# Kernel optimization log

Hardware: AMD Instinct MI355X
Metric: run time of the kernel (lower is better)

Reference implementation:

```python
import jax, jax.numpy as jnp
import numpy as np

B, L, HID = 16, 2048, 4096
CQ, CKV = 1536, 512
H, DH, DR = 32, 128, 64


def setup_inputs() -> dict:
    key = jax.random.key(0)
    ks = jax.random.split(key, 12)
    w = lambda k, shp: jax.random.normal(k, shp, dtype=jnp.float32) * 0.02
    return {
        'hidden_states': jax.random.normal(ks[0], (B, 1, HID), dtype=jnp.float32),
        'cached_cKV': jax.random.normal(ks[1], (B, L, CKV), dtype=jnp.float32),
        'cached_kR': jax.random.normal(ks[2], (B, L, H * DR), dtype=jnp.float32),
        'W_DQ': w(ks[3], (HID, CQ)),
        'W_DKV': w(ks[4], (HID, CKV)),
        'W_UQ_C': w(ks[5], (CQ, H * DH)),
        'W_UQ_R': w(ks[6], (CQ, H * DR)),
        'W_KR': w(ks[7], (HID, H * DR)),
        'W_UK_C': w(ks[8], (CKV, H * DH)),
        'W_UV_C': w(ks[9], (CKV, H * DH)),
        'W_O': w(ks[10], (H * DH, HID)),
    }


def _apply_rope(x, pos):
    # x: (B, S, H, D); standard rotate-pairs RoPE with base 10000
    D = x.shape[-1]
    inv_freq = 1.0 / (10000.0 ** (jnp.arange(0, D, 2, dtype=jnp.float32) / D))
    ang = pos.astype(jnp.float32)[:, None] * inv_freq[None, :]  # (S, D/2)
    cos = jnp.cos(ang)[None, :, None, :]
    sin = jnp.sin(ang)[None, :, None, :]
    x1, x2 = x[..., ::2], x[..., 1::2]
    r1 = x1 * cos - x2 * sin
    r2 = x1 * sin + x2 * cos
    return jnp.stack([r1, r2], axis=-1).reshape(x.shape)


def reference(hidden_states, cached_cKV, cached_kR, W_DQ, W_DKV, W_UQ_C, W_UQ_R, W_KR, W_UK_C, W_UV_C, W_O):
    b, seq_len, _ = hidden_states.shape  # seq_len == 1 (decode)
    # compressed query + up-projections
    cQ_t = jnp.einsum('bsh,hq->bsq', hidden_states, W_DQ)
    qC_t = jnp.einsum('bsq,qc->bsc', cQ_t, W_UQ_C)
    qR_t = jnp.einsum('bsq,qr->bsr', cQ_t, W_UQ_R)
    kR_t = jnp.einsum('bsh,hr->bsr', hidden_states, W_KR)
    # RoPE on rope-dim heads (single decode token -> position 0)
    pos = jnp.arange(seq_len)
    qR_t = _apply_rope(qR_t.reshape(b, seq_len, H, DR), pos).reshape(b, seq_len, H * DR)
    kR_t = _apply_rope(kR_t.reshape(b, seq_len, H, DR), pos).reshape(b, seq_len, H * DR)
    # compressed KV for new token
    cKV_t = jnp.einsum('bsh,hv->bsv', hidden_states, W_DKV)
    # absorption trick: fold W_UK_C into the query
    qC_eff = jnp.einsum('bsc,ck->bsk', qC_t, W_UK_C.T)  # (B,1,CKV)
    score_Cprefix = jnp.einsum('bsk,bLk->bsL', qC_eff, cached_cKV)
    new_token_score_C = jnp.einsum('bsk,bsk->bs', qC_eff, cKV_t)[:, None]
    score_Rprefix = jnp.einsum('bsr,bLr->bsL', qR_t, cached_kR)
    new_token_score_R = jnp.einsum('bsr,bsr->bs', qR_t, kR_t)[:, None]
    scores = jnp.concatenate([score_Cprefix + score_Rprefix,
                              new_token_score_C + new_token_score_R], axis=-1)
    scores = scores / jnp.sqrt(jnp.float32(DH + DR))
    attn_probs = jax.nn.softmax(scores, axis=-1)  # (B,1,L+1)
    # absorbed value/output projection
    W_VO = jnp.einsum('kv,vc->kc', W_UV_C, W_O)  # (CKV, HID)
    prefix_value = jnp.einsum('bLk,kc->bLc', cached_cKV, W_VO)
    prefix_value_agg = jnp.einsum('bsl,blc->bsc', attn_probs[..., :-1], prefix_value)
    new_value = jnp.einsum('bsk,kc->bsc', cKV_t, W_VO)
    output = prefix_value_agg + attn_probs[..., -1:] * new_value
    new_cached_cKV = jnp.concatenate([cached_cKV, cKV_t], axis=1)
    new_cached_kR = jnp.concatenate([cached_kR, kR_t], axis=1)
    return output, new_cached_cKV, new_cached_kR
```

## Files before the change

kernel.cpp:

```cpp
#include <hip/hip_runtime.h>

#define HIDN 4096
#define CQD  1536
#define CKVD 512
#define NH   32
#define DH   128
#define DR   64
#define BATCH 16
#define SEQL 2048
#define HDR  (NH*DR)
#define HDH  (NH*DH)
#define LP1  (SEQL+1)

__device__ __forceinline__ void gemm16_core(
    const float* __restrict__ A, int K, int k0, int KC,
    const float* __restrict__ W, int ldW, int wcol,
    float* __restrict__ C, int ldC, int ccol,
    float* sA, int tid) {
    for (int i = tid; i < KC * 16; i += 256) {
        int k = i >> 4, b = i & 15;
        sA[i] = A[b * K + k0 + k];
    }
    __syncthreads();
    float2 acc[16];
#pragma unroll
    for (int b = 0; b < 16; ++b) acc[b] = make_float2(0.f, 0.f);
    const float* Wp = W + (size_t)k0 * ldW + wcol;
    const float4* sA4 = (const float4*)sA;
#pragma unroll 4
    for (int k = 0; k < KC; ++k) {
        float2 w = *(const float2*)(Wp + (size_t)k * ldW);
        float av[16];
        *(float4*)&av[0]  = sA4[k * 4 + 0];
        *(float4*)&av[4]  = sA4[k * 4 + 1];
        *(float4*)&av[8]  = sA4[k * 4 + 2];
        *(float4*)&av[12] = sA4[k * 4 + 3];
#pragma unroll
        for (int b = 0; b < 16; ++b) {
            acc[b].x += av[b] * w.x;
            acc[b].y += av[b] * w.y;
        }
    }
#pragma unroll
    for (int b = 0; b < 16; ++b) {
        atomicAdd(&C[b * ldC + ccol],     acc[b].x);
        atomicAdd(&C[b * ldC + ccol + 1], acc[b].y);
    }
}

__global__ __launch_bounds__(256) void proj_hidden(
    const float* __restrict__ hidden,
    const float* __restrict__ W_DQ, const float* __restrict__ W_DKV,
    const float* __restrict__ W_KR,
    float* __restrict__ cQ, float* __restrict__ cKV_t, float* __restrict__ kR_t) {
    const int KC = 128;
    __shared__ float sA[16 * KC];
    int nb = blockIdx.x;
    const float* W; float* C; int ld; int col0;
    if (nb < 3)      { W = W_DQ;  C = cQ;    ld = CQD;  col0 = nb * 512; }
    else if (nb < 4) { W = W_DKV; C = cKV_t; ld = CKVD; col0 = 0; }
    else             { W = W_KR;  C = kR_t;  ld = HDR;  col0 = (nb - 4) * 512; }
    int cn = col0 + threadIdx.x * 2;
    gemm16_core(hidden, HIDN, blockIdx.y * KC, KC, W, ld, cn, C, ld, cn, sA, threadIdx.x);
}

__global__ __launch_bounds__(256) void proj_cq(
    const float* __restrict__ cQ,
    const float* __restrict__ W_UQ_C, const float* __restrict__ W_UQ_R,
    float* __restrict__ qC, float* __restrict__ qR) {
    const int KC = 64;
    __shared__ float sA[16 * KC];
    int nb = blockIdx.x;
    const float* W; float* C; int ld; int col0;
    if (nb < 8) { W = W_UQ_C; C = qC; ld = HDH; col0 = nb * 512; }
    else        { W = W_UQ_R; C = qR; ld = HDR; col0 = (nb - 8) * 512; }
    int cn = col0 + threadIdx.x * 2;
    gemm16_core(cQ, CQD, blockIdx.y * KC, KC, W, ld, cn, C, ld, cn, sA, threadIdx.x);
}

template <int KC>
__global__ __launch_bounds__(256) void gemm16_gen(
    const float* __restrict__ A, const float* __restrict__ W,
    float* __restrict__ C, int K, int N) {
    __shared__ float sA[16 * KC];
    int cn = blockIdx.x * 512 + threadIdx.x * 2;
    gemm16_core(A, K, blockIdx.y * KC, KC, W, N, cn, C, N, cn, sA, threadIdx.x);
}

__global__ __launch_bounds__(256) void qceff_v2(
    const float* __restrict__ qC, const float* __restrict__ WUK,
    float* __restrict__ qC_eff) {
    int wave = threadIdx.x >> 6, lane = threadIdx.x & 63;
    int k = blockIdx.x * 2 + (wave >> 1);
    int half = wave & 1;
    const float4* wrow = (const float4*)(WUK + (size_t)k * HDH + half * 2048);
    const float4* q4   = (const float4*)(qC + half * 2048);
    float acc[16];
#pragma unroll
    for (int b = 0; b < 16; ++b) acc[b] = 0.f;
#pragma unroll
    for (int it = 0; it < 8; ++it) {
        int c4 = it * 64 + lane;
        float4 w = wrow[c4];
#pragma unroll
        for (int b = 0; b < 16; ++b) {
            float4 q = q4[b * 1024 + c4];
            acc[b] += q.x * w.x + q.y * w.y + q.z * w.z + q.w * w.w;
        }
    }
#pragma unroll
    for (int b = 0; b < 16; ++b) {
        float v = acc[b];
#pragma unroll
        for (int off = 32; off > 0; off >>= 1) v += __shfl_down(v, off, 64);
        if (lane == 0) atomicAdd(&qC_eff[b * CKVD + k], v);
    }
}

__global__ __launch_bounds__(256) void score_copy_kernel(
    const float* __restrict__ cached_cKV, const float* __restrict__ cached_kR,
    const float* __restrict__ cKV_t, const float* __restrict__ kR_t,
    const float* __restrict__ qC_eff, const float* __restrict__ qR,
    float* __restrict__ out_cKV, float* __restrict__ out_kR,
    float* __restrict__ scores) {
    int l = blockIdx.x;
    int b = blockIdx.y;
    int tid = threadIdx.x;
    int wave = tid >> 6, lane = tid & 63;
    const float4* ckv_row;
    const float4* kr_row;
    if (l < SEQL) {
        ckv_row = (const float4*)(cached_cKV + ((size_t)b * SEQL + l) * CKVD);
        kr_row  = (const float4*)(cached_kR  + ((size_t)b * SEQL + l) * HDR);
    } else {
        ckv_row = (const float4*)(cKV_t + b * CKVD);
        kr_row  = (const float4*)(kR_t + b * HDR);
    }
    float4* oc  = (float4*)(out_cKV + ((size_t)b * LP1 + l) * CKVD);
    float4* okr = (float4*)(out_kR  + ((size_t)b * LP1 + l) * HDR);
    const float4* qc4 = (const float4*)(qC_eff + b * CKVD);
    const float4* qr4 = (const float4*)(qR + b * HDR);
    float acc = 0.f;
    if (tid < 128) {
        float4 v = ckv_row[tid];
        float4 q = qc4[tid];
        acc += v.x * q.x + v.y * q.y + v.z * q.z + v.w * q.w;
        oc[tid] = v;
    }
#pragma unroll
    for (int j = 0; j < 2; ++j) {
        int i = tid + j * 256;
        float4 v = kr_row[i];
        float4 q = qr4[i];
        acc += v.x * q.x + v.y * q.y + v.z * q.z + v.w * q.w;
        okr[i] = v;
    }
#pragma unroll
    for (int off = 32; off > 0; off >>= 1) acc += __shfl_down(acc, off, 64);
    __shared__ float sRed[4];
    if (lane == 0) sRed[wave] = acc;
    __syncthreads();
    if (tid == 0)
        scores[b * LP1 + l] =
            (sRed[0] + sRed[1] + sRed[2] + sRed[3]) * 0.07216878364870323f;
}

__global__ __launch_bounds__(256) void softmax_kernel(
    const float* __restrict__ scores, float* __restrict__ probs) {
    int b = blockIdx.x;
    int tid = threadIdx.x;
    __shared__ float red[256];
    float m = -1e30f;
    for (int i = tid; i < LP1; i += 256) m = fmaxf(m, scores[b * LP1 + i]);
    red[tid] = m; __syncthreads();
    for (int s = 128; s > 0; s >>= 1) {
        if (tid < s) red[tid] = fmaxf(red[tid], red[tid + s]);
        __syncthreads();
    }
    m = red[0]; __syncthreads();
    float sum = 0.f;
    for (int i = tid; i < LP1; i += 256) sum += __expf(scores[b * LP1 + i] - m);
    red[tid] = sum; __syncthreads();
    for (int s = 128; s > 0; s >>= 1) {
        if (tid < s) red[tid] += red[tid + s];
        __syncthreads();
    }
    float inv = 1.0f / red[0];
    for (int i = tid; i < LP1; i += 256)
        probs[b * LP1 + i] = __expf(scores[b * LP1 + i] - m) * inv;
}

__global__ __launch_bounds__(256) void ctx_kernel(
    const float* __restrict__ out_cKV, const float* __restrict__ probs,
    float* __restrict__ ctx) {
    int b = blockIdx.y;
    int tid = threadIdx.x;
    int c4 = tid & 127, sub = tid >> 7;
    int l0 = blockIdx.x * 128;
    int lend = l0 + 128; if (lend > LP1) lend = LP1;
    float4 acc = make_float4(0.f, 0.f, 0.f, 0.f);
    for (int l = l0 + sub; l < lend; l += 2) {
        float p = probs[b * LP1 + l];
        const float4* row = (const float4*)(out_cKV + ((size_t)b * LP1 + l) * CKVD);
        float4 v = row[c4];
        acc.x += p * v.x; acc.y += p * v.y; acc.z += p * v.z; acc.w += p * v.w;
    }
    float* dst = ctx + b * CKVD + c4 * 4;
    atomicAdd(dst + 0, acc.x);
    atomicAdd(dst + 1, acc.y);
    atomicAdd(dst + 2, acc.z);
    atomicAdd(dst + 3, acc.w);
}

extern "C" void kernel_launch(void* const* d_in, const int* in_sizes, int n_in,
                              void* d_out, int out_size, void* d_ws, size_t ws_size,
                              hipStream_t stream) {
    const float* hidden     = (const float*)d_in[0];
    const float* cached_cKV = (const float*)d_in[1];
    const float* cached_kR  = (const float*)d_in[2];
    const float* W_DQ   = (const float*)d_in[3];
    const float* W_DKV  = (const float*)d_in[4];
    const float* W_UQ_C = (const float*)d_in[5];
    const float* W_UQ_R = (const float*)d_in[6];
    const float* W_KR   = (const float*)d_in[7];
    const float* W_UK_C = (const float*)d_in[8];
    const float* W_UV_C = (const float*)d_in[9];
    const float* W_O    = (const float*)d_in[10];

    float* out     = (float*)d_out;
    float* out_cKV = out + BATCH * HDH;
    float* out_kR  = out_cKV + (size_t)BATCH * LP1 * CKVD;

    float* ws      = (float*)d_ws;
    float* cQ      = ws;
    float* cKV_t   = cQ + BATCH * CQD;
    float* kR_t    = cKV_t + BATCH * CKVD;
    float* qC      = kR_t + BATCH * HDR;
    float* qR      = qC + BATCH * HDH;
    float* qC_eff  = qR + BATCH * HDR;
    float* ctx     = qC_eff + BATCH * CKVD;
    float* tbuf    = ctx + BATCH * CKVD;
    float* scores  = tbuf + BATCH * HDH;
    float* probs   = scores + BATCH * LP1;
    size_t n_ws_floats = (size_t)(probs + BATCH * LP1 - ws);

    hipMemsetAsync(d_ws, 0, n_ws_floats * sizeof(float), stream);
    hipMemsetAsync(d_out, 0, (size_t)BATCH * HDH * sizeof(float), stream);

    dim3 blk(256);
    proj_hidden<<<dim3(8, HIDN / 128), blk, 0, stream>>>(
        hidden, W_DQ, W_DKV, W_KR, cQ, cKV_t, kR_t);
    proj_cq<<<dim3(12, CQD / 64), blk, 0, stream>>>(cQ, W_UQ_C, W_UQ_R, qC, qR);
    qceff_v2<<<dim3(CKVD / 2), blk, 0, stream>>>(qC, W_UK_C, qC_eff);
    score_copy_kernel<<<dim3(LP1, BATCH), blk, 0, stream>>>(
        cached_cKV, cached_kR, cKV_t, kR_t, qC_eff, qR, out_cKV, out_kR, scores);
    softmax_kernel<<<dim3(BATCH), blk, 0, stream>>>(scores, probs);
    ctx_kernel<<<dim3((LP1 + 127) / 128, BATCH), blk, 0, stream>>>(out_cKV, probs, ctx);
    gemm16_gen<32><<<dim3(HDH / 512, CKVD / 32), blk, 0, stream>>>(
        ctx, W_UV_C, tbuf, CKVD, HDH);
    gemm16_gen<128><<<dim3(HIDN / 512, HDH / 128), blk, 0, stream>>>(
        tbuf, W_O, out, HDH, HIDN);
}
```

Baseline: 790.2 us.

## Rework decode MLA kernels: narrower GEMM tiles, nontemporal copies, fused softmax into ctx

```diff
diff --git a/kernel.cpp b/kernel.cpp
--- a/kernel.cpp
+++ b/kernel.cpp
@@ -12,40 +12,43 @@
 #define HDH  (NH*DH)
 #define LP1  (SEQL+1)
 
-__device__ __forceinline__ void gemm16_core(
+typedef float f32x4 __attribute__((ext_vector_type(4)));
+
+__device__ __forceinline__ f32x4 nt_load4(const float* p) {
+    return __builtin_nontemporal_load((const f32x4*)p);
+}
+__device__ __forceinline__ void nt_store4(float* p, f32x4 v) {
+    __builtin_nontemporal_store(v, (f32x4*)p);
+}
+
+__device__ __forceinline__ void gemm16_col_core(
     const float* __restrict__ A, int K, int k0, int KC,
-    const float* __restrict__ W, int ldW, int wcol,
-    float* __restrict__ C, int ldC, int ccol,
+    const float* __restrict__ W, int ldW, int col,
+    float* __restrict__ C, int ldC,
     float* sA, int tid) {
     for (int i = tid; i < KC * 16; i += 256) {
         int k = i >> 4, b = i & 15;
         sA[i] = A[b * K + k0 + k];
     }
     __syncthreads();
-    float2 acc[16];
-#pragma unroll
-    for (int b = 0; b < 16; ++b) acc[b] = make_float2(0.f, 0.f);
-    const float* Wp = W + (size_t)k0 * ldW + wcol;
+    float acc[16];
+#pragma unroll
+    for (int b = 0; b < 16; ++b) acc[b] = 0.f;
+    const float* Wp = W + (size_t)k0 * ldW + col;
     const float4* sA4 = (const float4*)sA;
 #pragma unroll 4
     for (int k = 0; k < KC; ++k) {
-        float2 w = *(const float2*)(Wp + (size_t)k * ldW);
+        float w = Wp[(size_t)k * ldW];
         float av[16];
         *(float4*)&av[0]  = sA4[k * 4 + 0];
         *(float4*)&av[4]  = sA4[k * 4 + 1];
         *(float4*)&av[8]  = sA4[k * 4 + 2];
         *(float4*)&av[12] = sA4[k * 4 + 3];
 #pragma unroll
-        for (int b = 0; b < 16; ++b) {
-            acc[b].x += av[b] * w.x;
-            acc[b].y += av[b] * w.y;
-        }
-    }
-#pragma unroll
-    for (int b = 0; b < 16; ++b) {
-        atomicAdd(&C[b * ldC + ccol],     acc[b].x);
-        atomicAdd(&C[b * ldC + ccol + 1], acc[b].y);
-    }
+        for (int b = 0; b < 16; ++b) acc[b] += av[b] * w;
+    }
+#pragma unroll
+    for (int b = 0; b < 16; ++b) atomicAdd(&C[b * ldC + col], acc[b]);
 }
 
 __global__ __launch_bounds__(256) void proj_hidden(
@@ -57,11 +60,11 @@
     __shared__ float sA[16 * KC];
     int nb = blockIdx.x;
     const float* W; float* C; int ld; int col0;
-    if (nb < 3)      { W = W_DQ;  C = cQ;    ld = CQD;  col0 = nb * 512; }
-    else if (nb < 4) { W = W_DKV; C = cKV_t; ld = CKVD; col0 = 0; }
-    else             { W = W_KR;  C = kR_t;  ld = HDR;  col0 = (nb - 4) * 512; }
-    int cn = col0 + threadIdx.x * 2;
-    gemm16_core(hidden, HIDN, blockIdx.y * KC, KC, W, ld, cn, C, ld, cn, sA, threadIdx.x);
+    if (nb < 6)      { W = W_DQ;  C = cQ;    ld = CQD;  col0 = nb * 256; }
+    else if (nb < 8) { W = W_DKV; C = cKV_t; ld = CKVD; col0 = (nb - 6) * 256; }
+    else             { W = W_KR;  C = kR_t;  ld = HDR;  col0 = (nb - 8) * 256; }
+    gemm16_col_core(hidden, HIDN, blockIdx.y * KC, KC, W, ld,
+                    col0 + threadIdx.x, C, ld, sA, threadIdx.x);
 }
 
 __global__ __launch_bounds__(256) void proj_cq(
@@ -72,10 +75,10 @@
     __shared__ float sA[16 * KC];
     int nb = blockIdx.x;
     const float* W; float* C; int ld; int col0;
-    if (nb < 8) { W = W_UQ_C; C = qC; ld = HDH; col0 = nb * 512; }
-    else        { W = W_UQ_R; C = qR; ld = HDR; col0 = (nb - 8) * 512; }
-    int cn = col0 + threadIdx.x * 2;
-    gemm16_core(cQ, CQD, blockIdx.y * KC, KC, W, ld, cn, C, ld, cn, sA, threadIdx.x);
+    if (nb < 16) { W = W_UQ_C; C = qC; ld = HDH; col0 = nb * 256; }
+    else         { W = W_UQ_R; C = qR; ld = HDR; col0 = (nb - 16) * 256; }
+    gemm16_col_core(cQ, CQD, blockIdx.y * KC, KC, W, ld,
+                    col0 + threadIdx.x, C, ld, sA, threadIdx.x);
 }
 
 template <int KC>
@@ -83,24 +86,23 @@
     const float* __restrict__ A, const float* __restrict__ W,
     float* __restrict__ C, int K, int N) {
     __shared__ float sA[16 * KC];
-    int cn = blockIdx.x * 512 + threadIdx.x * 2;
-    gemm16_core(A, K, blockIdx.y * KC, KC, W, N, cn, C, N, cn, sA, threadIdx.x);
-}
-
-__global__ __launch_bounds__(256) void qceff_v2(
+    int col = blockIdx.x * 256 + threadIdx.x;
+    gemm16_col_core(A, K, blockIdx.y * KC, KC, W, N, col, C, N, sA, threadIdx.x);
+}
+
+__global__ __launch_bounds__(256) void qceff_v3(
     const float* __restrict__ qC, const float* __restrict__ WUK,
     float* __restrict__ qC_eff) {
-    int wave = threadIdx.x >> 6, lane = threadIdx.x & 63;
-    int k = blockIdx.x * 2 + (wave >> 1);
-    int half = wave & 1;
-    const float4* wrow = (const float4*)(WUK + (size_t)k * HDH + half * 2048);
-    const float4* q4   = (const float4*)(qC + half * 2048);
+    int k = blockIdx.x;
+    int tid = threadIdx.x, wave = tid >> 6, lane = tid & 63;
+    const float4* wrow = (const float4*)(WUK + (size_t)k * HDH);
+    const float4* q4   = (const float4*)qC;
     float acc[16];
 #pragma unroll
     for (int b = 0; b < 16; ++b) acc[b] = 0.f;
 #pragma unroll
-    for (int it = 0; it < 8; ++it) {
-        int c4 = it * 64 + lane;
+    for (int it = 0; it < 4; ++it) {
+        int c4 = wave * 256 + it * 64 + lane;
         float4 w = wrow[c4];
 #pragma unroll
         for (int b = 0; b < 16; ++b) {
@@ -108,13 +110,50 @@
             acc[b] += q.x * w.x + q.y * w.y + q.z * w.z + q.w * w.w;
         }
     }
+    __shared__ float sRed[64];
 #pragma unroll
     for (int b = 0; b < 16; ++b) {
         float v = acc[b];
 #pragma unroll
         for (int off = 32; off > 0; off >>= 1) v += __shfl_down(v, off, 64);
-        if (lane == 0) atomicAdd(&qC_eff[b * CKVD + k], v);
-    }
+        if (lane == 0) sRed[wave * 16 + b] = v;
+    }
+    __syncthreads();
+    if (tid < 16)
+        qC_eff[tid * CKVD + k] =
+            sRed[tid] + sRed[16 + tid] + sRed[32 + tid] + sRed[48 + tid];
+}
+
+__device__ __forceinline__ float score_copy_row(
+    int b, int l,
+    const float* __restrict__ cached_cKV, const float* __restrict__ cached_kR,
+    const float* __restrict__ cKV_t, const float* __restrict__ kR_t,
+    float* __restrict__ out_cKV, float* __restrict__ out_kR,
+    float4 qcv, float4 qrv0, float4 qrv1, int tid) {
+    const float* ckv_row;
+    const float* kr_row;
+    if (l < SEQL) {
+        ckv_row = cached_cKV + ((size_t)b * SEQL + l) * CKVD;
+        kr_row  = cached_kR  + ((size_t)b * SEQL + l) * HDR;
+    } else {
+        ckv_row = cKV_t + b * CKVD;
+        kr_row  = kR_t + b * HDR;
+    }
+    float* oc  = out_cKV + ((size_t)b * LP1 + l) * CKVD;
+    float* okr = out_kR  + ((size_t)b * LP1 + l) * HDR;
+    float acc = 0.f;
+    if (tid < 128) {
+        f32x4 v = nt_load4(ckv_row + tid * 4);
+        *(f32x4*)(oc + tid * 4) = v;
+        acc += v[0] * qcv.x + v[1] * qcv.y + v[2] * qcv.z + v[3] * qcv.w;
+    }
+    f32x4 v0 = nt_load4(kr_row + tid * 4);
+    nt_store4(okr + tid * 4, v0);
+    acc += v0[0] * qrv0.x + v0[1] * qrv0.y + v0[2] * qrv0.z + v0[3] * qrv0.w;
+    f32x4 v1 = nt_load4(kr_row + (tid + 256) * 4);
+    nt_store4(okr + (tid + 256) * 4, v1);
+    acc += v1[0] * qrv1.x + v1[1] * qrv1.y + v1[2] * qrv1.z + v1[3] * qrv1.w;
+    return acc;
 }
 
 __global__ __launch_bounds__(256) void score_copy_kernel(
@@ -123,50 +162,41 @@
     const float* __restrict__ qC_eff, const float* __restrict__ qR,
     float* __restrict__ out_cKV, float* __restrict__ out_kR,
     float* __restrict__ scores) {
-    int l = blockIdx.x;
     int b = blockIdx.y;
     int tid = threadIdx.x;
     int wave = tid >> 6, lane = tid & 63;
-    const float4* ckv_row;
-    const float4* kr_row;
-    if (l < SEQL) {
-        ckv_row = (const float4*)(cached_cKV + ((size_t)b * SEQL + l) * CKVD);
-        kr_row  = (const float4*)(cached_kR  + ((size_t)b * SEQL + l) * HDR);
-    } else {
-        ckv_row = (const float4*)(cKV_t + b * CKVD);
-        kr_row  = (const float4*)(kR_t + b * HDR);
-    }
-    float4* oc  = (float4*)(out_cKV + ((size_t)b * LP1 + l) * CKVD);
-    float4* okr = (float4*)(out_kR  + ((size_t)b * LP1 + l) * HDR);
+    int r0 = blockIdx.x * 2;
+    bool h1 = (r0 + 1 <= SEQL);
     const float4* qc4 = (const float4*)(qC_eff + b * CKVD);
     const float4* qr4 = (const float4*)(qR + b * HDR);
-    float acc = 0.f;
-    if (tid < 128) {
-        float4 v = ckv_row[tid];
-        float4 q = qc4[tid];
-        acc += v.x * q.x + v.y * q.y + v.z * q.z + v.w * q.w;
-        oc[tid] = v;
-    }
-#pragma unroll
-    for (int j = 0; j < 2; ++j) {
-        int i = tid + j * 256;
-        float4 v = kr_row[i];
-        float4 q = qr4[i];
-        acc += v.x * q.x + v.y * q.y + v.z * q.z + v.w * q.w;
-        okr[i] = v;
-    }
-#pragma unroll
-    for (int off = 32; off > 0; off >>= 1) acc += __shfl_down(acc, off, 64);
-    __shared__ float sRed[4];
-    if (lane == 0) sRed[wave] = acc;
+    float4 qcv = make_float4(0.f, 0.f, 0.f, 0.f);
+    if (tid < 128) qcv = qc4[tid];
+    float4 qrv0 = qr4[tid];
+    float4 qrv1 = qr4[tid + 256];
+
+    float acc0 = score_copy_row(b, r0, cached_cKV, cached_kR, cKV_t, kR_t,
+                                out_cKV, out_kR, qcv, qrv0, qrv1, tid);
+    float acc1 = 0.f;
+    if (h1)
+        acc1 = score_copy_row(b, r0 + 1, cached_cKV, cached_kR, cKV_t, kR_t,
+                              out_cKV, out_kR, qcv, qrv0, qrv1, tid);
+
+    __shared__ float sRed[2][4];
+#pragma unroll
+    for (int off = 32; off > 0; off >>= 1) acc0 += __shfl_down(acc0, off, 64);
+#pragma unroll
+    for (int off = 32; off > 0; off >>= 1) acc1 += __shfl_down(acc1, off, 64);
+    if (lane == 0) { sRed[0][wave] = acc0; sRed[1][wave] = acc1; }
     __syncthreads();
-    if (tid == 0)
-        scores[b * LP1 + l] =
-            (sRed[0] + sRed[1] + sRed[2] + sRed[3]) * 0.07216878364870323f;
-}
-
-__global__ __launch_bounds__(256) void softmax_kernel(
-    const float* __restrict__ scores, float* __restrict__ probs) {
+    int nrows = h1 ? 2 : 1;
+    if (tid < nrows)
+        scores[b * LP1 + r0 + tid] =
+            (sRed[tid][0] + sRed[tid][1] + sRed[tid][2] + sRed[tid][3]) *
+            0.07216878364870323f;
+}
+
+__global__ __launch_bounds__(256) void msum_kernel(
+    const float* __restrict__ scores, float* __restrict__ mz) {
     int b = blockIdx.x;
     int tid = threadIdx.x;
     __shared__ float red[256];
@@ -185,22 +215,21 @@
         if (tid < s) red[tid] += red[tid + s];
         __syncthreads();
     }
-    float inv = 1.0f / red[0];
-    for (int i = tid; i < LP1; i += 256)
-        probs[b * LP1 + i] = __expf(scores[b * LP1 + i] - m) * inv;
+    if (tid == 0) { mz[b * 2] = m; mz[b * 2 + 1] = 1.0f / red[0]; }
 }
 
 __global__ __launch_bounds__(256) void ctx_kernel(
-    const float* __restrict__ out_cKV, const float* __restrict__ probs,
-    float* __restrict__ ctx) {
+    const float* __restrict__ out_cKV, const float* __restrict__ scores,
+    const float* __restrict__ mz, float* __restrict__ ctx) {
     int b = blockIdx.y;
     int tid = threadIdx.x;
     int c4 = tid & 127, sub = tid >> 7;
-    int l0 = blockIdx.x * 128;
-    int lend = l0 + 128; if (lend > LP1) lend = LP1;
+    int l0 = blockIdx.x * 64;
+    int lend = l0 + 64; if (lend > LP1) lend = LP1;
+    float m = mz[b * 2], invZ = mz[b * 2 + 1];
     float4 acc = make_float4(0.f, 0.f, 0.f, 0.f);
     for (int l = l0 + sub; l < lend; l += 2) {
-        float p = probs[b * LP1 + l];
+        float p = __expf(scores[b * LP1 + l] - m) * invZ;
         const float4* row = (const float4*)(out_cKV + ((size_t)b * LP1 + l) * CKVD);
         float4 v = row[c4];
         acc.x += p * v.x; acc.y += p * v.y; acc.z += p * v.z; acc.w += p * v.w;
@@ -241,23 +270,24 @@
     float* ctx     = qC_eff + BATCH * CKVD;
     float* tbuf    = ctx + BATCH * CKVD;
     float* scores  = tbuf + BATCH * HDH;
-    float* probs   = scores + BATCH * LP1;
-    size_t n_ws_floats = (size_t)(probs + BATCH * LP1 - ws);
-
-    hipMemsetAsync(d_ws, 0, n_ws_floats * sizeof(float), stream);
+    float* mz      = scores + BATCH * LP1;
+
+    size_t n_zero = (size_t)(scores - ws);
+    hipMemsetAsync(d_ws, 0, n_zero * sizeof(float), stream);
     hipMemsetAsync(d_out, 0, (size_t)BATCH * HDH * sizeof(float), stream);
 
     dim3 blk(256);
-    proj_hidden<<<dim3(8, HIDN / 128), blk, 0, stream>>>(
+    proj_hidden<<<dim3(16, HIDN / 128), blk, 0, stream>>>(
         hidden, W_DQ, W_DKV, W_KR, cQ, cKV_t, kR_t);
-    proj_cq<<<dim3(12, CQD / 64), blk, 0, stream>>>(cQ, W_UQ_C, W_UQ_R, qC, qR);
-    qceff_v2<<<dim3(CKVD / 2), blk, 0, stream>>>(qC, W_UK_C, qC_eff);
-    score_copy_kernel<<<dim3(LP1, BATCH), blk, 0, stream>>>(
+    proj_cq<<<dim3(24, CQD / 64), blk, 0, stream>>>(cQ, W_UQ_C, W_UQ_R, qC, qR);
+    qceff_v3<<<dim3(CKVD), blk, 0, stream>>>(qC, W_UK_C, qC_eff);
+    score_copy_kernel<<<dim3(LP1 / 2 + 1, BATCH), blk, 0, stream>>>(
         cached_cKV, cached_kR, cKV_t, kR_t, qC_eff, qR, out_cKV, out_kR, scores);
-    softmax_kernel<<<dim3(BATCH), blk, 0, stream>>>(scores, probs);
-    ctx_kernel<<<dim3((LP1 + 127) / 128, BATCH), blk, 0, stream>>>(out_cKV, probs, ctx);
-    gemm16_gen<32><<<dim3(HDH / 512, CKVD / 32), blk, 0, stream>>>(
+    msum_kernel<<<dim3(BATCH), blk, 0, stream>>>(scores, mz);
+    ctx_kernel<<<dim3((LP1 + 63) / 64, BATCH), blk, 0, stream>>>(
+        out_cKV, scores, mz, ctx);
+    gemm16_gen<16><<<dim3(HDH / 256, CKVD / 16), blk, 0, stream>>>(
         ctx, W_UV_C, tbuf, CKVD, HDH);
-    gemm16_gen<128><<<dim3(HIDN / 512, HDH / 128), blk, 0, stream>>>(
+    gemm16_gen<128><<<dim3(HIDN / 256, HDH / 128), blk, 0, stream>>>(
         tbuf, W_O, out, HDH, HIDN);
 }
```

Result: faster. 732.8 us (-7.3%).
